# Optimization experiments

Measured on AMD Instinct MI355X. Metric: run time of the kernel, lower is better.

Reference implementation:

```python
import jax, jax.numpy as jnp
import numpy as np

EPS = 1e-7  # same clamp torch BCE effectively applies to avoid log(0)


def _level_bce(att, boxes, valid, area, level_id, H, W):
    # att: [B, h_l, w_l] predicted attention in (0,1); boxes: [B, N, 4]; valid/area: [B, N]
    B, hl, wl = att.shape
    base = 2.0 ** (level_id + 5)
    min_area = base * base * 0.5
    max_area = (base * 1.58) ** 2 * 2.0
    sel = valid & (area >= min_area) & (area <= max_area)  # [B, N]
    sx = wl / W
    sy = hl / H
    # rasterization bounds on the level grid (int() == floor for non-negative coords)
    x1 = jnp.maximum(jnp.floor(boxes[..., 0] * sx), 0.0)
    y1 = jnp.maximum(jnp.floor(boxes[..., 1] * sy), 0.0)
    x2 = jnp.minimum(jnp.ceil(boxes[..., 2] * sx) + 1.0, float(wl))
    y2 = jnp.minimum(jnp.ceil(boxes[..., 3] * sy) + 1.0, float(hl))
    rows = jnp.arange(hl, dtype=att.dtype)
    cols = jnp.arange(wl, dtype=att.dtype)
    # separable per-box row/col indicators -> matmul-style OR to avoid a [B,N,h,w] tensor
    rin = (sel[..., None] & (rows >= y1[..., None]) & (rows < y2[..., None])).astype(att.dtype)  # [B,N,h]
    cin = (sel[..., None] & (cols >= x1[..., None]) & (cols < x2[..., None])).astype(att.dtype)  # [B,N,w]
    mask_gt = (jnp.einsum('bnh,bnw->bhw', rin, cin) > 0).astype(att.dtype)  # [B,h,w]
    p = jnp.clip(att, EPS, 1.0 - EPS)
    bce = -(mask_gt * jnp.log(p) + (1.0 - mask_gt) * jnp.log1p(-p))
    return bce.mean(axis=(1, 2))  # [B]


def reference(att0, att1, att2, att3, att4, bboxs, h, w):
    atts = [att0, att1, att2, att3, att4]
    hf = float(h)
    wf = float(w)
    x1, y1, x2, y2, label = (bboxs[..., i] for i in range(5))
    valid = (label != -1) & (x1 <= wf) & (y1 <= hf) & (x2 <= wf) & (y2 <= hf)  # [B,N]
    area = (x2 - x1) * (y2 - y1)
    boxes = bboxs[..., :4]
    per_level = [
        _level_bce(a[:, 0, :, :], boxes, valid, area, i, hf, wf)
        for i, a in enumerate(atts)
    ]
    sample_loss = jnp.stack(per_level, axis=0).mean(axis=0)  # [B]
    has_box = valid.any(axis=1)
    sample_loss = jnp.where(has_box, sample_loss, jnp.zeros_like(sample_loss))
    return sample_loss.mean(keepdims=True)  # [1]


def setup_inputs() -> dict:
    key = jax.random.key(0)
    ks = jax.random.split(key, 10)
    B, N, H, W = 16, 96, 4096, 4096
    sizes = [(1024, 1024), (512, 512), (256, 256), (128, 128), (64, 64)]
    inp = {}
    for i, (hl, wl) in enumerate(sizes):
        inp[f'att{i}'] = jax.random.uniform(ks[i], (B, 1, hl, wl), jnp.float32, 1e-4, 1.0 - 1e-4)
    cx = jax.random.uniform(ks[5], (B, N), jnp.float32) * W
    cy = jax.random.uniform(ks[6], (B, N), jnp.float32) * H
    side = jnp.exp(jax.random.uniform(ks[7], (B, N), jnp.float32, np.log(24.0), np.log(1100.0)))
    x1 = jnp.clip(cx - side / 2, 0.0, float(W))
    x2 = jnp.clip(cx + side / 2, 0.0, float(W))
    y1 = jnp.clip(cy - side / 2, 0.0, float(H))
    y2 = jnp.clip(cy + side / 2, 0.0, float(H))
    label = jnp.where(jax.random.uniform(ks[8], (B, N), jnp.float32) < 0.1, -1.0, 1.0)
    inp['bboxs'] = jnp.stack([x1, y1, x2, y2, label], axis=-1)
    inp['h'] = H
    inp['w'] = W
    return inp
```

## Files before the change

kernel.cpp:

```cpp
#include <hip/hip_runtime.h>

#define B_SZ 16
#define N_BOX 96
#define EPSF 1e-7f

#define N_CORR   (B_SZ * 5)
#define N_STREAM 2736

__device__ __forceinline__ const float* pick_att(
    int l, const float* a0, const float* a1, const float* a2,
    const float* a3, const float* a4)
{
    switch (l) { case 0: return a0; case 1: return a1; case 2: return a2;
                 case 3: return a3; default: return a4; }
}

__device__ __forceinline__ float block_reduce(float s, float* wsum) {
    #pragma unroll
    for (int off = 32; off > 0; off >>= 1)
        s += __shfl_down(s, off, 64);
    int lane = threadIdx.x & 63, wv = threadIdx.x >> 6;
    if (lane == 0) wsum[wv] = s;
    __syncthreads();
    return wsum[0] + wsum[1] + wsum[2] + wsum[3];
}

__device__ __forceinline__ unsigned bits32(int lo, int hi) {
    unsigned top = (hi >= 32) ? 0xffffffffu : ((1u << hi) - 1u);
    return top & ~((1u << lo) - 1u);
}

__global__ __launch_bounds__(256)
void stream_kernel(const float* __restrict__ a0, const float* __restrict__ a1,
                   const float* __restrict__ a2, const float* __restrict__ a3,
                   const float* __restrict__ a4,
                   float* __restrict__ partial)
{
    __shared__ float wsum[4];
    int sbid = blockIdx.x;
    int l, start, bppShift;
    const float* att;
    if (sbid < 2048)      { l = 0; start = 0;    bppShift = 7; att = a0; }
    else if (sbid < 2560) { l = 1; start = 2048; bppShift = 5; att = a1; }
    else if (sbid < 2688) { l = 2; start = 2560; bppShift = 3; att = a2; }
    else if (sbid < 2720) { l = 3; start = 2688; bppShift = 1; att = a3; }
    else                  { l = 4; start = 2720; bppShift = 0; att = a4; }

    int planeF4 = 1 << (18 - 2 * l);
    int bil = sbid - start;
    int chunk = bil & ((1 << bppShift) - 1);
    int nf4 = planeF4 >> bppShift;
    unsigned gf4base = (unsigned)(bil >> bppShift) * (unsigned)planeF4
                     + (unsigned)chunk * (unsigned)nf4 + threadIdx.x;

    float s = 0.0f;
    if (nf4 == 2048) {
        float4 av[8];
        #pragma unroll
        for (int u = 0; u < 8; ++u)
            av[u] = reinterpret_cast<const float4*>(att)[gf4base + u * 256u];
        #pragma unroll
        for (int u = 0; u < 8; ++u) {
            float q0 = 1.0f - fminf(fmaxf(av[u].x, EPSF), 1.0f - EPSF);
            float q1 = 1.0f - fminf(fmaxf(av[u].y, EPSF), 1.0f - EPSF);
            float q2 = 1.0f - fminf(fmaxf(av[u].z, EPSF), 1.0f - EPSF);
            float q3 = 1.0f - fminf(fmaxf(av[u].w, EPSF), 1.0f - EPSF);
            s -= __logf((q0 * q1) * (q2 * q3));
        }
    } else {
        float4 av[4];
        #pragma unroll
        for (int u = 0; u < 4; ++u)
            av[u] = reinterpret_cast<const float4*>(att)[gf4base + u * 256u];
        #pragma unroll
        for (int u = 0; u < 4; ++u) {
            float q0 = 1.0f - fminf(fmaxf(av[u].x, EPSF), 1.0f - EPSF);
            float q1 = 1.0f - fminf(fmaxf(av[u].y, EPSF), 1.0f - EPSF);
            float q2 = 1.0f - fminf(fmaxf(av[u].z, EPSF), 1.0f - EPSF);
            float q3 = 1.0f - fminf(fmaxf(av[u].w, EPSF), 1.0f - EPSF);
            s -= __logf((q0 * q1) * (q2 * q3));
        }
    }

    float t = block_reduce(s, wsum);
    if (threadIdx.x == 0) partial[sbid] = t;
}

__global__ __launch_bounds__(256)
void corr_kernel(const float* __restrict__ a0, const float* __restrict__ a1,
                 const float* __restrict__ a2, const float* __restrict__ a3,
                 const float* __restrict__ a4,
                 const float* __restrict__ bboxs,
                 const int* __restrict__ hp, const int* __restrict__ wp,
                 float* __restrict__ corr)
{
    __shared__ int4 rect[N_BOX];
    __shared__ int Rcnt;
    __shared__ float wsum[4];

    int c = blockIdx.x;
    int b = c / 5, l = c % 5;
    const float* att = pick_att(l, a0, a1, a2, a3, a4);
    int wl = 1024 >> l;
    unsigned maxIdx = ((unsigned)B_SZ << (20 - 2 * l)) - 1u;
    float Wf = (float)(*wp), Hf = (float)(*hp);

    if (threadIdx.x == 0) Rcnt = 0;
    __syncthreads();

    if (threadIdx.x < N_BOX) {
        int n = threadIdx.x;
        const float* bx = bboxs + (b * N_BOX + n) * 5;
        float x1 = bx[0], y1 = bx[1], x2 = bx[2], y2 = bx[3], lb = bx[4];
        double based = (double)(32 << l);
        float mn  = (float)(based * based * 0.5);
        float mxv = (float)((based * 1.58) * (based * 1.58) * 2.0);
        float area = (x2 - x1) * (y2 - y1);
        bool ok = (lb != -1.0f) && (x1 <= Wf) && (y1 <= Hf) &&
                  (x2 <= Wf) && (y2 <= Hf) && (area >= mn) && (area <= mxv);
        float sx = (float)wl / Wf, sy = (float)wl / Hf;
        int ix1 = (int)fmaxf(floorf(x1 * sx), 0.0f);
        int iy1 = (int)fmaxf(floorf(y1 * sy), 0.0f);
        int ix2 = (int)fminf(ceilf(x2 * sx) + 1.0f, (float)wl);
        int iy2 = (int)fminf(ceilf(y2 * sy) + 1.0f, (float)wl);
        if (ok && ix2 > ix1 && iy2 > iy1) {
            int i = atomicAdd(&Rcnt, 1);
            rect[i] = make_int4(ix1, iy1, ix2, iy2);
        }
    }
    __syncthreads();

    int Rc = Rcnt;
    unsigned pbase = (unsigned)b << (20 - 2 * l);
    float s = 0.0f;

    for (int pair = (int)threadIdx.x; pair < Rc * 32; pair += 256) {
        int r = pair >> 5, row = pair & 31;
        int4 rc = rect[r];
        int wpx = rc.z - rc.x;
        for (int y = rc.y + row; y < rc.w; y += 32) {
            unsigned rowbase = pbase + (unsigned)y * (unsigned)wl + (unsigned)rc.x;
            for (int xoff = 0; xoff < wpx; xoff += 32) {
                unsigned m = bits32(0, min(wpx - xoff, 32));
                for (int q = 0; q < r; ++q) {
                    int4 qc = rect[q];
                    bool inRow = (y >= qc.y) && (y < qc.w);
                    int ql = max(qc.x - rc.x - xoff, 0);
                    int qh = min(qc.z - rc.x - xoff, 32);
                    if (inRow && ql < qh) m &= ~bits32(ql, qh);
                }
                if (!m) continue;
                float px[32];
                #pragma unroll
                for (int i = 0; i < 32; ++i) {
                    unsigned a = rowbase + (unsigned)(xoff + i);
                    px[i] = att[a < maxIdx ? a : maxIdx];
                }
                #pragma unroll
                for (int i = 0; i < 32; ++i) {
                    float wt = (float)((m >> i) & 1u);
                    float p = fminf(fmaxf(px[i], EPSF), 1.0f - EPSF);
                    s = fmaf(wt, __logf((1.0f - p) / p), s);
                }
            }
        }
    }

    float t = block_reduce(s, wsum);
    if (threadIdx.x == 0) corr[c] = t;
}

__global__ __launch_bounds__(256)
void finalize_kernel(const float* __restrict__ bboxs,
                     const int* __restrict__ hp, const int* __restrict__ wp,
                     const float* __restrict__ partial,
                     const float* __restrict__ corr,
                     float* __restrict__ out)
{
    __shared__ int hasbox[B_SZ];
    __shared__ double red[256];
    if (threadIdx.x < B_SZ) hasbox[threadIdx.x] = 0;
    __syncthreads();
    float Wf = (float)(*wp), Hf = (float)(*hp);
    for (int i = (int)threadIdx.x; i < B_SZ * N_BOX; i += 256) {
        const float* bx = bboxs + i * 5;
        if (bx[4] != -1.0f && bx[0] <= Wf && bx[1] <= Hf && bx[2] <= Wf && bx[3] <= Hf)
            hasbox[i / N_BOX] = 1;
    }
    __syncthreads();

    double t = 0.0;
    for (int i = (int)threadIdx.x; i < N_STREAM; i += 256) {
        int l, start, bppShift;
        if (i < 2048)      { l = 0; start = 0;    bppShift = 7; }
        else if (i < 2560) { l = 1; start = 2048; bppShift = 5; }
        else if (i < 2688) { l = 2; start = 2560; bppShift = 3; }
        else if (i < 2720) { l = 3; start = 2688; bppShift = 1; }
        else               { l = 4; start = 2720; bppShift = 0; }
        int b = (i - start) >> bppShift;
        if (hasbox[b]) {
            int wl = 1024 >> l;
            t += (double)partial[i] / (double)(wl * wl);
        }
    }
    for (int i = (int)threadIdx.x; i < N_CORR; i += 256) {
        int b = i / 5, l = i % 5;
        if (hasbox[b]) {
            int wl = 1024 >> l;
            t += (double)corr[i] / (double)(wl * wl);
        }
    }
    red[threadIdx.x] = t;
    __syncthreads();
    for (int off = 128; off > 0; off >>= 1) {
        if ((int)threadIdx.x < off) red[threadIdx.x] += red[threadIdx.x + off];
        __syncthreads();
    }
    if (threadIdx.x == 0)
        out[0] = (float)(red[0] / (5.0 * (double)B_SZ));
}

extern "C" void kernel_launch(void* const* d_in, const int* in_sizes, int n_in,
                              void* d_out, int out_size, void* d_ws, size_t ws_size,
                              hipStream_t stream)
{
    const float* a0 = (const float*)d_in[0];
    const float* a1 = (const float*)d_in[1];
    const float* a2 = (const float*)d_in[2];
    const float* a3 = (const float*)d_in[3];
    const float* a4 = (const float*)d_in[4];
    const float* bboxs = (const float*)d_in[5];
    const int* hp = (const int*)d_in[6];
    const int* wp = (const int*)d_in[7];

    float* partial = (float*)d_ws;
    float* corr    = partial + N_STREAM;

    stream_kernel<<<N_STREAM, 256, 0, stream>>>(a0, a1, a2, a3, a4, partial);
    corr_kernel<<<N_CORR, 256, 0, stream>>>(a0, a1, a2, a3, a4,
                                            bboxs, hp, wp, corr);
    finalize_kernel<<<1, 256, 0, stream>>>(bboxs, hp, wp, partial, corr,
                                           (float*)d_out);
}
```

Baseline: 50.92 us.

## Fuse stream and correction kernels into one launch; batch logs in correction

Merges the dense BCE streaming kernel and the per-box correction kernel into a single grid. The 80 correction blocks come first so they can overlap with the bandwidth-bound streaming blocks, and one launch plus its inter-kernel gap goes away. The correction inner loop now multiplies four masked odds ratios together and takes one log per group instead of one per pixel, which cuts transcendental work. The grouped product can lose precision or overflow for extreme probabilities, and the fused kernel's shared-memory and register use is the union of both paths, which may lower occupancy.

```diff
diff --git a/kernel.cpp b/kernel.cpp
--- a/kernel.cpp
+++ b/kernel.cpp
@@ -6,6 +6,7 @@
 
 #define N_CORR   (B_SZ * 5)
 #define N_STREAM 2736
+#define N_BLOCKS (N_CORR + N_STREAM)
 
 __device__ __forceinline__ const float* pick_att(
     int l, const float* a0, const float* a1, const float* a2,
@@ -31,74 +32,71 @@
 }
 
 __global__ __launch_bounds__(256)
-void stream_kernel(const float* __restrict__ a0, const float* __restrict__ a1,
-                   const float* __restrict__ a2, const float* __restrict__ a3,
-                   const float* __restrict__ a4,
-                   float* __restrict__ partial)
+void fused_kernel(const float* __restrict__ a0, const float* __restrict__ a1,
+                  const float* __restrict__ a2, const float* __restrict__ a3,
+                  const float* __restrict__ a4,
+                  const float* __restrict__ bboxs,
+                  const int* __restrict__ hp, const int* __restrict__ wp,
+                  float* __restrict__ partial,
+                  float* __restrict__ corr)
 {
     __shared__ float wsum[4];
-    int sbid = blockIdx.x;
-    int l, start, bppShift;
-    const float* att;
-    if (sbid < 2048)      { l = 0; start = 0;    bppShift = 7; att = a0; }
-    else if (sbid < 2560) { l = 1; start = 2048; bppShift = 5; att = a1; }
-    else if (sbid < 2688) { l = 2; start = 2560; bppShift = 3; att = a2; }
-    else if (sbid < 2720) { l = 3; start = 2688; bppShift = 1; att = a3; }
-    else                  { l = 4; start = 2720; bppShift = 0; att = a4; }
-
-    int planeF4 = 1 << (18 - 2 * l);
-    int bil = sbid - start;
-    int chunk = bil & ((1 << bppShift) - 1);
-    int nf4 = planeF4 >> bppShift;
-    unsigned gf4base = (unsigned)(bil >> bppShift) * (unsigned)planeF4
-                     + (unsigned)chunk * (unsigned)nf4 + threadIdx.x;
-
+    int bid = blockIdx.x;
     float s = 0.0f;
-    if (nf4 == 2048) {
-        float4 av[8];
-        #pragma unroll
-        for (int u = 0; u < 8; ++u)
-            av[u] = reinterpret_cast<const float4*>(att)[gf4base + u * 256u];
-        #pragma unroll
-        for (int u = 0; u < 8; ++u) {
-            float q0 = 1.0f - fminf(fmaxf(av[u].x, EPSF), 1.0f - EPSF);
-            float q1 = 1.0f - fminf(fmaxf(av[u].y, EPSF), 1.0f - EPSF);
-            float q2 = 1.0f - fminf(fmaxf(av[u].z, EPSF), 1.0f - EPSF);
-            float q3 = 1.0f - fminf(fmaxf(av[u].w, EPSF), 1.0f - EPSF);
-            s -= __logf((q0 * q1) * (q2 * q3));
-        }
-    } else {
-        float4 av[4];
-        #pragma unroll
-        for (int u = 0; u < 4; ++u)
-            av[u] = reinterpret_cast<const float4*>(att)[gf4base + u * 256u];
-        #pragma unroll
-        for (int u = 0; u < 4; ++u) {
-            float q0 = 1.0f - fminf(fmaxf(av[u].x, EPSF), 1.0f - EPSF);
-            float q1 = 1.0f - fminf(fmaxf(av[u].y, EPSF), 1.0f - EPSF);
-            float q2 = 1.0f - fminf(fmaxf(av[u].z, EPSF), 1.0f - EPSF);
-            float q3 = 1.0f - fminf(fmaxf(av[u].w, EPSF), 1.0f - EPSF);
-            s -= __logf((q0 * q1) * (q2 * q3));
-        }
-    }
-
-    float t = block_reduce(s, wsum);
-    if (threadIdx.x == 0) partial[sbid] = t;
-}
-
-__global__ __launch_bounds__(256)
-void corr_kernel(const float* __restrict__ a0, const float* __restrict__ a1,
-                 const float* __restrict__ a2, const float* __restrict__ a3,
-                 const float* __restrict__ a4,
-                 const float* __restrict__ bboxs,
-                 const int* __restrict__ hp, const int* __restrict__ wp,
-                 float* __restrict__ corr)
-{
+
+    if (bid >= N_CORR) {
+        int sbid = bid - N_CORR;
+        int l, start, bppShift;
+        const float* att;
+        if (sbid < 2048)      { l = 0; start = 0;    bppShift = 7; att = a0; }
+        else if (sbid < 2560) { l = 1; start = 2048; bppShift = 5; att = a1; }
+        else if (sbid < 2688) { l = 2; start = 2560; bppShift = 3; att = a2; }
+        else if (sbid < 2720) { l = 3; start = 2688; bppShift = 1; att = a3; }
+        else                  { l = 4; start = 2720; bppShift = 0; att = a4; }
+
+        int planeF4 = 1 << (18 - 2 * l);
+        int bil = sbid - start;
+        int chunk = bil & ((1 << bppShift) - 1);
+        int nf4 = planeF4 >> bppShift;
+        unsigned gf4base = (unsigned)(bil >> bppShift) * (unsigned)planeF4
+                         + (unsigned)chunk * (unsigned)nf4 + threadIdx.x;
+
+        if (nf4 == 2048) {
+            float4 av[8];
+            #pragma unroll
+            for (int u = 0; u < 8; ++u)
+                av[u] = reinterpret_cast<const float4*>(att)[gf4base + u * 256u];
+            #pragma unroll
+            for (int u = 0; u < 8; ++u) {
+                float q0 = 1.0f - fminf(fmaxf(av[u].x, EPSF), 1.0f - EPSF);
+                float q1 = 1.0f - fminf(fmaxf(av[u].y, EPSF), 1.0f - EPSF);
+                float q2 = 1.0f - fminf(fmaxf(av[u].z, EPSF), 1.0f - EPSF);
+                float q3 = 1.0f - fminf(fmaxf(av[u].w, EPSF), 1.0f - EPSF);
+                s -= __logf((q0 * q1) * (q2 * q3));
+            }
+        } else {
+            float4 av[4];
+            #pragma unroll
+            for (int u = 0; u < 4; ++u)
+                av[u] = reinterpret_cast<const float4*>(att)[gf4base + u * 256u];
+            #pragma unroll
+            for (int u = 0; u < 4; ++u) {
+                float q0 = 1.0f - fminf(fmaxf(av[u].x, EPSF), 1.0f - EPSF);
+                float q1 = 1.0f - fminf(fmaxf(av[u].y, EPSF), 1.0f - EPSF);
+                float q2 = 1.0f - fminf(fmaxf(av[u].z, EPSF), 1.0f - EPSF);
+                float q3 = 1.0f - fminf(fmaxf(av[u].w, EPSF), 1.0f - EPSF);
+                s -= __logf((q0 * q1) * (q2 * q3));
+            }
+        }
+        float t = block_reduce(s, wsum);
+        if (threadIdx.x == 0) partial[sbid] = t;
+        return;
+    }
+
     __shared__ int4 rect[N_BOX];
     __shared__ int Rcnt;
-    __shared__ float wsum[4];
-
-    int c = blockIdx.x;
+
+    int c = bid;
     int b = c / 5, l = c % 5;
     const float* att = pick_att(l, a0, a1, a2, a3, a4);
     int wl = 1024 >> l;
@@ -132,7 +130,6 @@
 
     int Rc = Rcnt;
     unsigned pbase = (unsigned)b << (20 - 2 * l);
-    float s = 0.0f;
 
     for (int pair = (int)threadIdx.x; pair < Rc * 32; pair += 256) {
         int r = pair >> 5, row = pair & 31;
@@ -157,10 +154,15 @@
                     px[i] = att[a < maxIdx ? a : maxIdx];
                 }
                 #pragma unroll
-                for (int i = 0; i < 32; ++i) {
-                    float wt = (float)((m >> i) & 1u);
-                    float p = fminf(fmaxf(px[i], EPSF), 1.0f - EPSF);
-                    s = fmaf(wt, __logf((1.0f - p) / p), s);
+                for (int i = 0; i < 32; i += 4) {
+                    float g = 1.0f;
+                    #pragma unroll
+                    for (int j = 0; j < 4; ++j) {
+                        float p = fminf(fmaxf(px[i + j], EPSF), 1.0f - EPSF);
+                        float ratio = (1.0f - p) / p;
+                        g *= ((m >> (i + j)) & 1u) ? ratio : 1.0f;
+                    }
+                    if (g != 1.0f) s += __logf(g);
                 }
             }
         }
@@ -236,9 +238,8 @@
     float* partial = (float*)d_ws;
     float* corr    = partial + N_STREAM;
 
-    stream_kernel<<<N_STREAM, 256, 0, stream>>>(a0, a1, a2, a3, a4, partial);
-    corr_kernel<<<N_CORR, 256, 0, stream>>>(a0, a1, a2, a3, a4,
-                                            bboxs, hp, wp, corr);
+    fused_kernel<<<N_BLOCKS, 256, 0, stream>>>(a0, a1, a2, a3, a4,
+                                               bboxs, hp, wp, partial, corr);
     finalize_kernel<<<1, 256, 0, stream>>>(bboxs, hp, wp, partial, corr,
                                            (float*)d_out);
 }
```

After: 41.54 us. 1.23x faster.
